# Optimization experiments

Hardware: AMD Instinct MI355X
Metric: run time of the kernel (lower is better)

Reference implementation:

```python
import math
import jax, jax.numpy as jnp
import numpy as np

B, S, E, H = 4, 2048, 2048, 16
D = E // H
EPSILON, DELTA, MAX_GRAD_NORM = 1.0, 1e-05, 1.0
# Gaussian mechanism calibration: sigma = C * sqrt(2 ln(1.25/delta)) / epsilon
NOISE_SCALE = MAX_GRAD_NORM * math.sqrt(2.0 * math.log(1.25 / DELTA)) / EPSILON


def _xavier(key, fan_in, fan_out):
    lim = math.sqrt(6.0 / (fan_in + fan_out))
    return jax.random.uniform(key, (fan_out, fan_in), jnp.float32, -lim, lim)


def setup_inputs() -> dict:
    key = jax.random.key(0)
    ks = jax.random.split(key, 8)
    return {
        'query': jax.random.normal(ks[0], (B, S, E), jnp.float32),
        'key_t': jax.random.normal(ks[1], (B, S, E), jnp.float32),
        'value': jax.random.normal(ks[2], (B, S, E), jnp.float32),
        'Wq': _xavier(ks[3], E, E), 'bq': jnp.zeros((E,), jnp.float32),
        'Wk': _xavier(ks[4], E, E), 'bk': jnp.zeros((E,), jnp.float32),
        'Wv': _xavier(ks[5], E, E), 'bv': jnp.zeros((E,), jnp.float32),
        'Wo': _xavier(ks[6], E, E), 'bo': jnp.zeros((E,), jnp.float32),
        'noise': jax.random.normal(ks[7], (B, S, E), jnp.float32),
    }


def reference(query, key_t, value, Wq, bq, Wk, bk, Wv, bv, Wo, bo, noise):
    b, s, e = query.shape
    scale = 1.0 / math.sqrt(D)
    # QKV projections (torch Linear: x @ W.T + b) -> [b, s, H, D]
    q = (query @ Wq.T + bq).reshape(b, s, H, D)
    k = (key_t @ Wk.T + bk).reshape(b, s, H, D)
    v = (value @ Wv.T + bv).reshape(b, s, H, D)
    # attention scores [b, H, s, s]
    scores = jnp.einsum('bqhd,bkhd->bhqk', q, k) * scale
    attn = jax.nn.softmax(scores, axis=-1)
    ctx = jnp.einsum('bhqk,bkhd->bqhd', attn, v).reshape(b, s, e)
    # DP noise injected inside the kernel on the attention output
    ctx = ctx + noise * NOISE_SCALE
    # output projection
    return ctx @ Wo.T + bo
```

## Files before the change

kernel.cpp:

```cpp
#include <hip/hip_runtime.h>
#include <cmath>

#define BATCH 4
#define SEQ   2048
#define EMB   2048
#define NH    16
#define HD    128
#define MDIM  (BATCH*SEQ)
#define KDIM  EMB
#define NDIM  EMB

typedef __bf16 bf16x8 __attribute__((ext_vector_type(8)));
typedef float  f32x4  __attribute__((ext_vector_type(4)));

__device__ __forceinline__ ushort bf16rne(float f) {
  unsigned u = __builtin_bit_cast(unsigned, f);
  u += 0x7fffu + ((u >> 16) & 1u);
  return (ushort)(u >> 16);
}

__global__ __launch_bounds__(256) void cvt_bf16(const float* __restrict__ in,
                                                ushort* __restrict__ out) {
  int i = (blockIdx.x * 256 + threadIdx.x) * 4;
  float4 v = *(const float4*)(in + i);
  ushort4 o;
  o.x = bf16rne(v.x); o.y = bf16rne(v.y); o.z = bf16rne(v.z); o.w = bf16rne(v.w);
  *(ushort4*)(out + i) = o;
}

template<int MODE>
__global__ __launch_bounds__(256, 2)
void gemm_nt(const ushort* __restrict__ A, const ushort* __restrict__ Bm,
             const float* __restrict__ bias, void* __restrict__ out) {
  __shared__ ushort As[128][72];
  __shared__ ushort Bs[128][72];

  const int tid  = threadIdx.x;
  const int wave = tid >> 6, lane = tid & 63;
  const int l15  = lane & 15, quad = lane >> 4;
  const int m0 = blockIdx.x * 128, n0 = blockIdx.y * 128;
  const int wr = (wave >> 1) * 64, wc = (wave & 1) * 64;

  const f32x4 zero4 = {0.f, 0.f, 0.f, 0.f};
  f32x4 acc[4][4];
#pragma unroll
  for (int i = 0; i < 4; ++i)
#pragma unroll
    for (int j = 0; j < 4; ++j) acc[i][j] = zero4;

  for (int kk = 0; kk < KDIM; kk += 64) {
#pragma unroll
    for (int it = 0; it < 4; ++it) {
      int L = it * 256 + tid;
      int row = L >> 3, c8 = (L & 7) * 8;
      int4 va = *(const int4*)(A  + (size_t)(m0 + row) * KDIM + kk + c8);
      int4 vb = *(const int4*)(Bm + (size_t)(n0 + row) * KDIM + kk + c8);
      *(int4*)(&As[row][c8]) = va;
      *(int4*)(&Bs[row][c8]) = vb;
    }
    __syncthreads();
#pragma unroll
    for (int ks = 0; ks < 2; ++ks) {
      bf16x8 af[4], bfr[4];
#pragma unroll
      for (int i = 0; i < 4; ++i)
        af[i] = __builtin_bit_cast(bf16x8, *(const int4*)(&As[wr + i*16 + l15][ks*32 + quad*8]));
#pragma unroll
      for (int j = 0; j < 4; ++j)
        bfr[j] = __builtin_bit_cast(bf16x8, *(const int4*)(&Bs[wc + j*16 + l15][ks*32 + quad*8]));
#pragma unroll
      for (int i = 0; i < 4; ++i)
#pragma unroll
        for (int j = 0; j < 4; ++j)
          acc[i][j] = __builtin_amdgcn_mfma_f32_16x16x32_bf16(af[i], bfr[j], acc[i][j], 0, 0, 0);
    }
    __syncthreads();
  }

  if constexpr (MODE == 0) {
    float* O = (float*)out;
#pragma unroll
    for (int i = 0; i < 4; ++i)
#pragma unroll
      for (int j = 0; j < 4; ++j) {
        int n = n0 + wc + j*16 + l15;
        float bb = bias[n];
#pragma unroll
        for (int r = 0; r < 4; ++r) {
          int m = m0 + wr + i*16 + quad*4 + r;
          O[(size_t)m * NDIM + n] = acc[i][j][r] + bb;
        }
      }
  } else if constexpr (MODE == 1) {
    ushort* O = (ushort*)out;
#pragma unroll
    for (int i = 0; i < 4; ++i)
#pragma unroll
      for (int j = 0; j < 4; ++j) {
        int n = n0 + wc + j*16 + l15;
        float bb = bias[n];
        int h = n >> 7, d = n & 127;
#pragma unroll
        for (int r = 0; r < 4; ++r) {
          int m = m0 + wr + i*16 + quad*4 + r;
          int b = m >> 11, srow = m & 2047;
          O[(((size_t)(b*NH + h) * SEQ + srow) << 7) + d] = bf16rne(acc[i][j][r] + bb);
        }
      }
  } else {
    __shared__ float Tt[4][16][17];
    ushort* O = (ushort*)out;
    const int h = n0 >> 7;
#pragma unroll
    for (int i = 0; i < 4; ++i)
#pragma unroll
      for (int j = 0; j < 4; ++j) {
        int n = n0 + wc + j*16 + l15;
        float bb = bias[n];
#pragma unroll
        for (int r = 0; r < 4; ++r)
          Tt[wave][l15][quad*4 + r] = acc[i][j][r] + bb;
#pragma unroll
        for (int r = 0; r < 4; ++r) {
          int dl = quad*4 + r, sl = l15;
          float v = Tt[wave][dl][sl];
          int m = m0 + wr + i*16 + sl;
          int b = m >> 11, srow = m & 2047;
          int d = wc + j*16 + dl;
          O[((size_t)(b*NH + h) * HD + d) * SEQ + srow] = bf16rne(v);
        }
      }
  }
}

__global__ __launch_bounds__(256, 2)
void attn_kernel(const ushort* __restrict__ Qh, const ushort* __restrict__ Kh,
                 const ushort* __restrict__ Vt, const float* __restrict__ noise,
                 ushort* __restrict__ ctxn, float scale, float ns) {
  __shared__ ushort Ks[64 * 128];
  __shared__ ushort Vs[128 * 64];
  __shared__ ushort Ps[64 * 64];

  const int tid  = threadIdx.x;
  const int wave = tid >> 6, lane = tid & 63;
  const int l15  = lane & 15, quad = lane >> 4;
  const int q0 = blockIdx.x * 64;
  const int bh = blockIdx.y;
  const int b  = bh >> 4, h = bh & 15;

  bf16x8 qf[4];
  {
    const int qrow = q0 + wave*16 + l15;
    const ushort* qp = Qh + ((size_t)bh * SEQ + qrow) * HD;
#pragma unroll
    for (int ks = 0; ks < 4; ++ks)
      qf[ks] = __builtin_bit_cast(bf16x8, *(const int4*)(qp + ks*32 + quad*8));
  }

  const f32x4 zero4 = {0.f, 0.f, 0.f, 0.f};
  f32x4 o[8];
#pragma unroll
  for (int nb = 0; nb < 8; ++nb) o[nb] = zero4;
  float rs[4] = {0.f, 0.f, 0.f, 0.f};

  for (int k0 = 0; k0 < SEQ; k0 += 64) {
#pragma unroll
    for (int it = 0; it < 4; ++it) {
      int L = it * 256 + tid;
      int r = L >> 4, c8 = (L & 15) * 8;
      int4 v = *(const int4*)(Kh + ((size_t)bh * SEQ + k0 + r) * HD + c8);
      *(int4*)(&Ks[r * 128 + (c8 ^ ((r & 7) << 3))]) = v;
    }
#pragma unroll
    for (int it = 0; it < 4; ++it) {
      int L = it * 256 + tid;
      int r = L >> 3, c8 = (L & 7) * 8;
      int4 v = *(const int4*)(Vt + ((size_t)bh * HD + r) * SEQ + k0 + c8);
      *(int4*)(&Vs[r * 64 + (c8 ^ ((r & 7) << 3))]) = v;
    }
    __syncthreads();

#pragma unroll
    for (int ct = 0; ct < 4; ++ct) {
      f32x4 s = zero4;
      const int kr = ct*16 + l15;
      __builtin_amdgcn_s_setprio(1);
#pragma unroll
      for (int ks = 0; ks < 4; ++ks) {
        bf16x8 kf = __builtin_bit_cast(bf16x8,
            *(const int4*)(&Ks[kr * 128 + ((ks*32 + quad*8) ^ ((kr & 7) << 3))]));
        s = __builtin_amdgcn_mfma_f32_16x16x32_bf16(qf[ks], kf, s, 0, 0, 0);
      }
      __builtin_amdgcn_s_setprio(0);
#pragma unroll
      for (int r = 0; r < 4; ++r) {
        float p = __expf(s[r] * scale);
        rs[r] += p;
        int pr = wave*16 + quad*4 + r;
        int pc = ct*16 + l15;
        Ps[pr * 64 + (pc ^ ((pr & 7) << 3))] = bf16rne(p);
      }
    }

    __builtin_amdgcn_s_setprio(1);
#pragma unroll
    for (int ks2 = 0; ks2 < 2; ++ks2) {
      const int par = wave*16 + l15;
      bf16x8 pa = __builtin_bit_cast(bf16x8,
          *(const int4*)(&Ps[par * 64 + ((ks2*32 + quad*8) ^ ((par & 7) << 3))]));
#pragma unroll
      for (int nb = 0; nb < 8; ++nb) {
        const int vr = nb*16 + l15;
        bf16x8 vb = __builtin_bit_cast(bf16x8,
            *(const int4*)(&Vs[vr * 64 + ((ks2*32 + quad*8) ^ ((vr & 7) << 3))]));
        o[nb] = __builtin_amdgcn_mfma_f32_16x16x32_bf16(pa, vb, o[nb], 0, 0, 0);
      }
    }
    __builtin_amdgcn_s_setprio(0);
    __syncthreads();
  }

#pragma unroll
  for (int r = 0; r < 4; ++r) {
    float v = rs[r];
    v += __shfl_xor(v, 1);
    v += __shfl_xor(v, 2);
    v += __shfl_xor(v, 4);
    v += __shfl_xor(v, 8);
    rs[r] = v;
  }

#pragma unroll
  for (int r = 0; r < 4; ++r) {
    float inv = 1.0f / rs[r];
    int sg = q0 + wave*16 + quad*4 + r;
    size_t rowbase = ((size_t)(b * SEQ + sg)) * EMB + h * HD;
#pragma unroll
    for (int nb = 0; nb < 8; ++nb) {
      int e = nb*16 + l15;
      float val = o[nb][r] * inv + noise[rowbase + e] * ns;
      ctxn[rowbase + e] = bf16rne(val);
    }
  }
}

extern "C" void kernel_launch(void* const* d_in, const int* in_sizes, int n_in,
                              void* d_out, int out_size, void* d_ws, size_t ws_size,
                              hipStream_t stream) {
  const float* query = (const float*)d_in[0];
  const float* key_t = (const float*)d_in[1];
  const float* value = (const float*)d_in[2];
  const float* Wq = (const float*)d_in[3];
  const float* bq = (const float*)d_in[4];
  const float* Wk = (const float*)d_in[5];
  const float* bk = (const float*)d_in[6];
  const float* Wv = (const float*)d_in[7];
  const float* bv = (const float*)d_in[8];
  const float* Wo = (const float*)d_in[9];
  const float* bo = (const float*)d_in[10];
  const float* noise = (const float*)d_in[11];

  const size_t SZ_ACT = (size_t)MDIM * KDIM * 2;
  const size_t SZ_W   = (size_t)NDIM * KDIM * 2;
  const size_t need_full = 7 * SZ_ACT + 4 * SZ_W;

  char* p = (char*)d_ws;
  ushort *qb, *kb;
  if (ws_size >= need_full) {
    qb = (ushort*)p; p += SZ_ACT;
    kb = (ushort*)p; p += SZ_ACT;
  } else {
    qb = (ushort*)d_out;
    kb = (ushort*)((char*)d_out + SZ_ACT);
  }
  ushort* vb   = (ushort*)p; p += SZ_ACT;
  ushort* wqb  = (ushort*)p; p += SZ_W;
  ushort* wkb  = (ushort*)p; p += SZ_W;
  ushort* wvb  = (ushort*)p; p += SZ_W;
  ushort* wob  = (ushort*)p; p += SZ_W;
  ushort* Qh   = (ushort*)p; p += SZ_ACT;
  ushort* Kh   = (ushort*)p; p += SZ_ACT;
  ushort* Vt   = (ushort*)p; p += SZ_ACT;
  ushort* ctxn = (ushort*)p; p += SZ_ACT;

  const int nAct = MDIM * KDIM;
  const int nW   = NDIM * KDIM;
  const float NS = (float)sqrt(2.0 * log(1.25 / 1e-5));
  const float SCALE = (float)(1.0 / sqrt((double)HD));

  cvt_bf16<<<dim3(nAct / 1024), dim3(256), 0, stream>>>(query, qb);
  cvt_bf16<<<dim3(nAct / 1024), dim3(256), 0, stream>>>(key_t, kb);
  cvt_bf16<<<dim3(nAct / 1024), dim3(256), 0, stream>>>(value, vb);
  cvt_bf16<<<dim3(nW / 1024),   dim3(256), 0, stream>>>(Wq, wqb);
  cvt_bf16<<<dim3(nW / 1024),   dim3(256), 0, stream>>>(Wk, wkb);
  cvt_bf16<<<dim3(nW / 1024),   dim3(256), 0, stream>>>(Wv, wvb);
  cvt_bf16<<<dim3(nW / 1024),   dim3(256), 0, stream>>>(Wo, wob);

  dim3 ggrid(MDIM / 128, NDIM / 128);
  gemm_nt<1><<<ggrid, dim3(256), 0, stream>>>(qb, wqb, bq, (void*)Qh);
  gemm_nt<1><<<ggrid, dim3(256), 0, stream>>>(kb, wkb, bk, (void*)Kh);
  gemm_nt<2><<<ggrid, dim3(256), 0, stream>>>(vb, wvb, bv, (void*)Vt);

  attn_kernel<<<dim3(SEQ / 64, BATCH * NH), dim3(256), 0, stream>>>(
      Qh, Kh, Vt, noise, ctxn, SCALE, NS);

  gemm_nt<0><<<ggrid, dim3(256), 0, stream>>>(ctxn, wob, bo, d_out);
}
```

Before: 865.6 us.

## Double-buffer GEMM and attention tiles via direct global-to-LDS loads

Replaces register-staged global loads into shared memory with global_load_lds direct transfers and adds a second LDS buffer in both the projection GEMM and the attention kernel. The next K/V or A/B tile is issued before computing on the current one, so memory latency overlaps with MFMA work. The GEMM drops its padded rows, which may bring back LDS bank conflicts on fragment reads. The doubled LDS footprint may lower occupancy, and correctness depends on the loads completing before the end-of-iteration barrier.

```diff
diff --git a/kernel.cpp b/kernel.cpp
--- a/kernel.cpp
+++ b/kernel.cpp
@@ -19,6 +19,12 @@
   return (ushort)(u >> 16);
 }
 
+__device__ __forceinline__ void gld_lds16(const ushort* g, ushort* l) {
+  __builtin_amdgcn_global_load_lds(
+      (const __attribute__((address_space(1))) unsigned int*)g,
+      (__attribute__((address_space(3))) unsigned int*)l, 16, 0, 0);
+}
+
 __global__ __launch_bounds__(256) void cvt_bf16(const float* __restrict__ in,
                                                 ushort* __restrict__ out) {
   int i = (blockIdx.x * 256 + threadIdx.x) * 4;
@@ -32,8 +38,8 @@
 __global__ __launch_bounds__(256, 2)
 void gemm_nt(const ushort* __restrict__ A, const ushort* __restrict__ Bm,
              const float* __restrict__ bias, void* __restrict__ out) {
-  __shared__ ushort As[128][72];
-  __shared__ ushort Bs[128][72];
+  __shared__ ushort As[2][128 * 64];
+  __shared__ ushort Bs[2][128 * 64];
 
   const int tid  = threadIdx.x;
   const int wave = tid >> 6, lane = tid & 63;
@@ -48,26 +54,37 @@
 #pragma unroll
     for (int j = 0; j < 4; ++j) acc[i][j] = zero4;
 
+  const int srow = tid >> 3, sc8 = (tid & 7) * 8;
+  const int Lw   = tid & ~63;
+
+  auto STAGE = [&](int buf, int kk) {
+#pragma unroll
+    for (int it = 0; it < 4; ++it) {
+      gld_lds16(A  + (size_t)(m0 + it*32 + srow) * KDIM + kk + sc8,
+                &As[buf][(it*256 + Lw) * 8]);
+      gld_lds16(Bm + (size_t)(n0 + it*32 + srow) * KDIM + kk + sc8,
+                &Bs[buf][(it*256 + Lw) * 8]);
+    }
+  };
+
+  STAGE(0, 0);
+  __syncthreads();
+  int cur = 0;
   for (int kk = 0; kk < KDIM; kk += 64) {
-#pragma unroll
-    for (int it = 0; it < 4; ++it) {
-      int L = it * 256 + tid;
-      int row = L >> 3, c8 = (L & 7) * 8;
-      int4 va = *(const int4*)(A  + (size_t)(m0 + row) * KDIM + kk + c8);
-      int4 vb = *(const int4*)(Bm + (size_t)(n0 + row) * KDIM + kk + c8);
-      *(int4*)(&As[row][c8]) = va;
-      *(int4*)(&Bs[row][c8]) = vb;
-    }
-    __syncthreads();
+    if (kk + 64 < KDIM) STAGE(cur ^ 1, kk + 64);
+    const ushort* Ab = As[cur];
+    const ushort* Bb = Bs[cur];
 #pragma unroll
     for (int ks = 0; ks < 2; ++ks) {
       bf16x8 af[4], bfr[4];
 #pragma unroll
       for (int i = 0; i < 4; ++i)
-        af[i] = __builtin_bit_cast(bf16x8, *(const int4*)(&As[wr + i*16 + l15][ks*32 + quad*8]));
+        af[i] = __builtin_bit_cast(bf16x8,
+                  *(const int4*)(Ab + (wr + i*16 + l15) * 64 + ks*32 + quad*8));
 #pragma unroll
       for (int j = 0; j < 4; ++j)
-        bfr[j] = __builtin_bit_cast(bf16x8, *(const int4*)(&Bs[wc + j*16 + l15][ks*32 + quad*8]));
+        bfr[j] = __builtin_bit_cast(bf16x8,
+                  *(const int4*)(Bb + (wc + j*16 + l15) * 64 + ks*32 + quad*8));
 #pragma unroll
       for (int i = 0; i < 4; ++i)
 #pragma unroll
@@ -75,6 +92,7 @@
           acc[i][j] = __builtin_amdgcn_mfma_f32_16x16x32_bf16(af[i], bfr[j], acc[i][j], 0, 0, 0);
     }
     __syncthreads();
+    cur ^= 1;
   }
 
   if constexpr (MODE == 0) {
@@ -103,12 +121,12 @@
 #pragma unroll
         for (int r = 0; r < 4; ++r) {
           int m = m0 + wr + i*16 + quad*4 + r;
-          int b = m >> 11, srow = m & 2047;
-          O[(((size_t)(b*NH + h) * SEQ + srow) << 7) + d] = bf16rne(acc[i][j][r] + bb);
+          int b = m >> 11, srow2 = m & 2047;
+          O[(((size_t)(b*NH + h) * SEQ + srow2) << 7) + d] = bf16rne(acc[i][j][r] + bb);
         }
       }
   } else {
-    __shared__ float Tt[4][16][17];
+    float* TtF = (float*)&As[0][0];
     ushort* O = (ushort*)out;
     const int h = n0 >> 7;
 #pragma unroll
@@ -119,15 +137,15 @@
         float bb = bias[n];
 #pragma unroll
         for (int r = 0; r < 4; ++r)
-          Tt[wave][l15][quad*4 + r] = acc[i][j][r] + bb;
+          TtF[(wave*16 + l15)*17 + quad*4 + r] = acc[i][j][r] + bb;
 #pragma unroll
         for (int r = 0; r < 4; ++r) {
           int dl = quad*4 + r, sl = l15;
-          float v = Tt[wave][dl][sl];
+          float v = TtF[(wave*16 + dl)*17 + sl];
           int m = m0 + wr + i*16 + sl;
-          int b = m >> 11, srow = m & 2047;
+          int b = m >> 11, srow2 = m & 2047;
           int d = wc + j*16 + dl;
-          O[((size_t)(b*NH + h) * HD + d) * SEQ + srow] = bf16rne(v);
+          O[((size_t)(b*NH + h) * HD + d) * SEQ + srow2] = bf16rne(v);
         }
       }
   }
@@ -137,8 +155,8 @@
 void attn_kernel(const ushort* __restrict__ Qh, const ushort* __restrict__ Kh,
                  const ushort* __restrict__ Vt, const float* __restrict__ noise,
                  ushort* __restrict__ ctxn, float scale, float ns) {
-  __shared__ ushort Ks[64 * 128];
-  __shared__ ushort Vs[128 * 64];
+  __shared__ ushort Ks[2][64 * 128];
+  __shared__ ushort Vs[2][128 * 64];
   __shared__ ushort Ps[64 * 64];
 
   const int tid  = threadIdx.x;
@@ -148,6 +166,24 @@
   const int bh = blockIdx.y;
   const int b  = bh >> 4, h = bh & 15;
 
+  const ushort* Kb = Kh + (size_t)bh * SEQ * HD;
+  const ushort* Vb = Vt + (size_t)bh * HD * SEQ;
+
+  const int rkr = tid >> 4, rks = tid & 15;
+  const int rvr = tid >> 3, rvs = tid & 7;
+  const int Lw  = tid & ~63;
+
+  auto STAGE = [&](int buf, int k0) {
+#pragma unroll
+    for (int it = 0; it < 4; ++it)
+      gld_lds16(Kb + (size_t)(k0 + it*16 + rkr) * HD + (rks ^ (rkr & 7)) * 8,
+                &Ks[buf][(it*256 + Lw) * 8]);
+#pragma unroll
+    for (int it = 0; it < 4; ++it)
+      gld_lds16(Vb + (size_t)(it*32 + rvr) * SEQ + k0 + (rvs ^ (rvr & 7)) * 8,
+                &Vs[buf][(it*256 + Lw) * 8]);
+  };
+
   bf16x8 qf[4];
   {
     const int qrow = q0 + wave*16 + l15;
@@ -163,22 +199,13 @@
   for (int nb = 0; nb < 8; ++nb) o[nb] = zero4;
   float rs[4] = {0.f, 0.f, 0.f, 0.f};
 
+  STAGE(0, 0);
+  __syncthreads();
+  int cur = 0;
   for (int k0 = 0; k0 < SEQ; k0 += 64) {
-#pragma unroll
-    for (int it = 0; it < 4; ++it) {
-      int L = it * 256 + tid;
-      int r = L >> 4, c8 = (L & 15) * 8;
-      int4 v = *(const int4*)(Kh + ((size_t)bh * SEQ + k0 + r) * HD + c8);
-      *(int4*)(&Ks[r * 128 + (c8 ^ ((r & 7) << 3))]) = v;
-    }
-#pragma unroll
-    for (int it = 0; it < 4; ++it) {
-      int L = it * 256 + tid;
-      int r = L >> 3, c8 = (L & 7) * 8;
-      int4 v = *(const int4*)(Vt + ((size_t)bh * HD + r) * SEQ + k0 + c8);
-      *(int4*)(&Vs[r * 64 + (c8 ^ ((r & 7) << 3))]) = v;
-    }
-    __syncthreads();
+    if (k0 + 64 < SEQ) STAGE(cur ^ 1, k0 + 64);
+    const ushort* Kc = Ks[cur];
+    const ushort* Vc = Vs[cur];
 
 #pragma unroll
     for (int ct = 0; ct < 4; ++ct) {
@@ -188,7 +215,7 @@
 #pragma unroll
       for (int ks = 0; ks < 4; ++ks) {
         bf16x8 kf = __builtin_bit_cast(bf16x8,
-            *(const int4*)(&Ks[kr * 128 + ((ks*32 + quad*8) ^ ((kr & 7) << 3))]));
+            *(const int4*)(Kc + kr * 128 + ((ks*32 + quad*8) ^ ((kr & 7) << 3))));
         s = __builtin_amdgcn_mfma_f32_16x16x32_bf16(qf[ks], kf, s, 0, 0, 0);
       }
       __builtin_amdgcn_s_setprio(0);
@@ -212,12 +239,13 @@
       for (int nb = 0; nb < 8; ++nb) {
         const int vr = nb*16 + l15;
         bf16x8 vb = __builtin_bit_cast(bf16x8,
-            *(const int4*)(&Vs[vr * 64 + ((ks2*32 + quad*8) ^ ((vr & 7) << 3))]));
+            *(const int4*)(Vc + vr * 64 + ((ks2*32 + quad*8) ^ ((vr & 7) << 3))));
         o[nb] = __builtin_amdgcn_mfma_f32_16x16x32_bf16(pa, vb, o[nb], 0, 0, 0);
       }
     }
     __builtin_amdgcn_s_setprio(0);
     __syncthreads();
+    cur ^= 1;
   }
 
 #pragma unroll
```

After: 1.003 ms. 15.9% more time.
